# Performance work log

Measured on AMD Instinct MI355X. Metric: run time of the kernel, lower is better.

## Reference

```python
import jax, jax.numpy as jnp
import numpy as np

FEATURE_NUM = 2048
TEMPERATURE = 0.5
EPS = 1e-12


def setup_inputs() -> dict:
    key = jax.random.key(0)
    k1, k2 = jax.random.split(key)
    B, N = 8192, FEATURE_NUM
    f1 = jax.random.uniform(k1, (B, N), dtype=jnp.float32)
    f2 = jax.random.uniform(k2, (B, N), dtype=jnp.float32)
    return {"f1": f1, "f2": f2}


def reference(f1, f2):
    N = FEATURE_NUM
    K = 2 * N
    # rows = features, cols = batch samples
    f = jnp.concatenate([f1.T, f2.T], axis=0)  # [K, B]

    # normalized entropy loss (predictions are sigmoid outputs in (0,1))
    ent = -f * jnp.log(f + EPS) - (1.0 - f) * jnp.log(1.0 - f + EPS)
    neloss = jnp.mean(ent) / jnp.log(2.0)

    # L2 normalize rows (torch F.normalize: x / max(||x||, eps))
    norm = jnp.linalg.norm(f, axis=1, keepdims=True)
    fn = f / jnp.maximum(norm, EPS)

    sim = (fn @ fn.T) / TEMPERATURE  # [K, K]

    # positives: off-diagonals at +/- N
    pos = jnp.concatenate([jnp.diagonal(sim, N), jnp.diagonal(sim, -N)])  # [K]

    # logits per row = [pos, negatives]; negatives = row minus main diag and +/-N diag.
    # logsumexp(pos U negatives) == logsumexp over the row excluding only the main diagonal,
    # since pos IS the +/-N diagonal entry of that row.
    diag_mask = jnp.eye(K, dtype=bool)
    lse = jax.nn.logsumexp(jnp.where(diag_mask, -jnp.inf, sim), axis=1)  # [K]

    # cross-entropy with label 0 (the positive slot), mean reduction
    ce = jnp.mean(lse - pos)
    return ce - neloss
```

## Files before the change

### kernel.cpp

```cpp
#include <hip/hip_runtime.h>
#include <math.h>

typedef __attribute__((ext_vector_type(4))) float f32x4;
typedef __attribute__((ext_vector_type(8))) short short8;
typedef unsigned int u32;

#define B_DIM 8192
#define N_FEAT 2048
#define K_ROWS 4096
#define INV_T 2.0f
#define EPSF 1e-12f

#define GT 96
#define GGRID 43
#define NTILES 946

#define FT_OFF    0ull
#define NORM2_OFF 67108864ull
#define INV_OFF   (NORM2_OFF + 16384)
#define SUMSQ_OFF (INV_OFF + 16384)
#define RSUM_OFF  (SUMSQ_OFF + 16384)
#define PDOT_OFF  (RSUM_OFF + 16384)
#define ENT_OFF   (PDOT_OFF + 8192)
#define WS_END    (ENT_OFF + 2048)

__device__ __forceinline__ unsigned short f2bf(float x) {
  u32 u = __float_as_uint(x);
  u32 r = (u + 0x7fffu + ((u >> 16) & 1u)) >> 16;
  return (unsigned short)r;
}

__device__ __forceinline__ void gload16(const void* g, void* l) {
  __builtin_amdgcn_global_load_lds((const __attribute__((address_space(1))) u32*)g,
                                   (__attribute__((address_space(3))) u32*)l, 16, 0, 0);
}

__global__ __launch_bounds__(256) void stats_kernel(
    const float* __restrict__ f1, const float* __restrict__ f2,
    float* __restrict__ norm2, float* __restrict__ posdot,
    double* __restrict__ entpart) {
  const int col = blockIdx.x * 256 + threadIdx.x;
  const size_t base = (size_t)blockIdx.y * 64 * N_FEAT + col;
  const float* p1 = f1 + base;
  const float* p2 = f2 + base;
  float n1 = 0.f, n2 = 0.f, pd = 0.f, e0 = 0.f, e1 = 0.f;
#pragma unroll 8
  for (int r = 0; r < 64; ++r) {
    const float x = p1[(size_t)r * N_FEAT];
    const float y = p2[(size_t)r * N_FEAT];
    n1 += x * x; n2 += y * y; pd += x * y;
    e0 -= x * __log2f(x + EPSF) + (1.f - x) * __log2f(1.f - x + EPSF);
    e1 -= y * __log2f(y + EPSF) + (1.f - y) * __log2f(1.f - y + EPSF);
  }
  atomicAdd(&norm2[col], n1);
  atomicAdd(&norm2[N_FEAT + col], n2);
  atomicAdd(&posdot[col], pd);
  float ent = e0 + e1;
#pragma unroll
  for (int off = 1; off < 64; off <<= 1) ent += __shfl_xor(ent, off);
  if ((threadIdx.x & 63) == 0)
    atomicAdd(&entpart[(blockIdx.y * 8 + blockIdx.x + (threadIdx.x >> 6) * 64) & 255],
              (double)ent);
}

__global__ __launch_bounds__(256) void transpose_kernel(
    const float* __restrict__ f1, const float* __restrict__ f2,
    unsigned short* __restrict__ fT) {
  __shared__ float T1[64][65];
  __shared__ float T2[64][65];
  const int b0 = blockIdx.x * 64, k0 = blockIdx.y * 64;
  const int t = threadIdx.x;
  const int kq = t & 15, br = t >> 4;
#pragma unroll
  for (int rr = 0; rr < 4; ++rr) {
    const int b = br + rr * 16;
    const f32x4 v1 = *(const f32x4*)&f1[(size_t)(b0 + b) * N_FEAT + k0 + kq * 4];
    const f32x4 v2 = *(const f32x4*)&f2[(size_t)(b0 + b) * N_FEAT + k0 + kq * 4];
#pragma unroll
    for (int c = 0; c < 4; ++c) { T1[b][kq * 4 + c] = v1[c]; T2[b][kq * 4 + c] = v2[c]; }
  }
  __syncthreads();
  const int kl = t >> 2;
  const int b8 = (t & 3) * 16;
  short8 o0, o1;
#pragma unroll
  for (int j = 0; j < 8; ++j)  o0[j] = (short)f2bf(T1[b8 + j][kl]);
#pragma unroll
  for (int j = 8; j < 16; ++j) o1[j - 8] = (short)f2bf(T1[b8 + j][kl]);
  size_t gi = (size_t)(k0 + kl);
  *(short8*)&fT[gi * B_DIM + b0 + b8] = o0;
  *(short8*)&fT[gi * B_DIM + b0 + b8 + 8] = o1;
#pragma unroll
  for (int j = 0; j < 8; ++j)  o0[j] = (short)f2bf(T2[b8 + j][kl]);
#pragma unroll
  for (int j = 8; j < 16; ++j) o1[j - 8] = (short)f2bf(T2[b8 + j][kl]);
  gi = (size_t)(N_FEAT + k0 + kl);
  *(short8*)&fT[gi * B_DIM + b0 + b8] = o0;
  *(short8*)&fT[gi * B_DIM + b0 + b8 + 8] = o1;
}

__global__ void inv_kernel(const float* __restrict__ norm2, float* __restrict__ inv) {
  const int i = blockIdx.x * 256 + threadIdx.x;
  if (i < K_ROWS) inv[i] = 1.f / fmaxf(sqrtf(norm2[i]), EPSF);
}

__global__ __launch_bounds__(256, 4) void gram_kernel(
    const unsigned short* __restrict__ fT, const float* __restrict__ inv,
    float* __restrict__ rowsum) {
  __shared__ __align__(16) unsigned short Al[GT * 64];
  __shared__ __align__(16) unsigned short Bl[GT * 64];
  const int orig = blockIdx.x;
  const int xcd = orig & 7;
  const int bid = (xcd < 2 ? xcd * 119 : 238 + (xcd - 2) * 118) + (orig >> 3);
  int r = (int)((sqrtf(8.f * (float)bid + 1.f) - 1.f) * 0.5f);
  while ((r + 1) * (r + 2) / 2 <= bid) ++r;
  while (r * (r + 1) / 2 > bid) --r;
  const int tj = r, ti = bid - r * (r + 1) / 2;

  const int t = threadIdx.x, lane = t & 63, wave = t >> 6;
  const int wr = wave >> 1, wc = wave & 1;
  const int Rb = wr * 48, Cb = wc * 48;
  const int rowl = lane & 15, lhi = lane >> 4;
  const int srow8 = wave * 8 + (lane >> 3);
  const int scol = (lane & 7) * 8;
  const int tb = ti * GT, tjb = tj * GT;
  const bool diagT = (ti == tj);

  const unsigned short* pa[3];
  const unsigned short* pb[3];
#pragma unroll
  for (int it = 0; it < 3; ++it) {
    int ra = tb + it * 32 + srow8;  ra = ra < K_ROWS - 1 ? ra : K_ROWS - 1;
    int rb2 = tjb + it * 32 + srow8; rb2 = rb2 < K_ROWS - 1 ? rb2 : K_ROWS - 1;
    pa[it] = fT + (size_t)ra * B_DIM + scol;
    pb[it] = fT + (size_t)rb2 * B_DIM + scol;
  }

  f32x4 acc[3][3];
  const f32x4 zero = {0.f, 0.f, 0.f, 0.f};
#pragma unroll
  for (int m = 0; m < 3; ++m)
#pragma unroll
    for (int n = 0; n < 3; ++n) acc[m][n] = zero;

  for (int kt = 0; kt < B_DIM / 64; ++kt) {
    const size_t ko = (size_t)kt * 64;
#pragma unroll
    for (int it = 0; it < 3; ++it) {
      gload16(pa[it] + ko, &Al[(it * 32 + wave * 8) * 64]);
      gload16(pb[it] + ko, &Bl[(it * 32 + wave * 8) * 64]);
    }
    asm volatile("s_waitcnt vmcnt(0)" ::: "memory");
    __syncthreads();
#pragma unroll
    for (int kk = 0; kk < 64; kk += 32) {
      short8 af[3], bfv[3];
      const int kc = kk + lhi * 8;
#pragma unroll
      for (int m = 0; m < 3; ++m)
        af[m] = *(const short8*)&Al[(Rb + m * 16 + rowl) * 64 + kc];
#pragma unroll
      for (int n = 0; n < 3; ++n)
        bfv[n] = *(const short8*)&Bl[(Cb + n * 16 + rowl) * 64 + kc];
#pragma unroll
      for (int m = 0; m < 3; ++m)
#pragma unroll
        for (int n = 0; n < 3; ++n)
          acc[m][n] = __builtin_amdgcn_mfma_f32_16x16x32_bf16(af[m], bfv[n], acc[m][n], 0, 0, 0);
    }
    __syncthreads();
  }

  float invj[3];
  bool cval[3];
#pragma unroll
  for (int n = 0; n < 3; ++n) {
    const int cg = tjb + Cb + n * 16 + rowl;
    cval[n] = cg < K_ROWS;
    invj[n] = inv[cg < K_ROWS ? cg : K_ROWS - 1];
  }
#pragma unroll
  for (int m = 0; m < 3; ++m) {
#pragma unroll
    for (int rg = 0; rg < 4; ++rg) {
      const int rloc = Rb + m * 16 + lhi * 4 + rg;
      const int rgl = tb + rloc;
      const bool rv = rgl < K_ROWS;
      const float invi = inv[rv ? rgl : K_ROWS - 1];
#pragma unroll
      for (int n = 0; n < 3; ++n) {
        const int cloc = Cb + n * 16 + rowl;
        const float e = __expf(acc[m][n][rg] * invi * invj[n] * INV_T);
        const bool keep = rv && cval[n] && !(diagT && rloc == cloc);
        acc[m][n][rg] = keep ? e : 0.f;
      }
    }
  }
#pragma unroll
  for (int m = 0; m < 3; ++m) {
#pragma unroll
    for (int rg = 0; rg < 4; ++rg) {
      float s = acc[m][0][rg] + acc[m][1][rg] + acc[m][2][rg];
      s += __shfl_xor(s, 1); s += __shfl_xor(s, 2);
      s += __shfl_xor(s, 4); s += __shfl_xor(s, 8);
      if (rowl == 0) {
        const int rgl = tb + Rb + m * 16 + lhi * 4 + rg;
        if (rgl < K_ROWS) atomicAdd(&rowsum[rgl], s);
      }
    }
  }
  if (!diagT) {
#pragma unroll
    for (int n = 0; n < 3; ++n) {
      float s = 0.f;
#pragma unroll
      for (int m = 0; m < 3; ++m)
#pragma unroll
        for (int rg = 0; rg < 4; ++rg) s += acc[m][n][rg];
      s += __shfl_xor(s, 16); s += __shfl_xor(s, 32);
      if (lhi == 0) {
        const int cg = tjb + Cb + n * 16 + rowl;
        if (cg < K_ROWS) atomicAdd(&rowsum[cg], s);
      }
    }
  }
}

__global__ __launch_bounds__(256) void final_kernel(
    const float* __restrict__ rowsum,
    const float* __restrict__ inv, const float* __restrict__ posdot,
    const double* __restrict__ entpart, float* __restrict__ out) {
  __shared__ double red[4];
  __shared__ double rede[4];
  const int t = threadIdx.x, lane = t & 63, wave = t >> 6;
  double ssum = 0.0;
  for (int i = t; i < K_ROWS; i += 256) {
    const float invi = inv[i];
    const float lse = __logf(rowsum[i]);
    const int ip = (i < N_FEAT) ? i : i - N_FEAT;
    const int io = (i < N_FEAT) ? i + N_FEAT : i - N_FEAT;
    const float pos = posdot[ip] * invi * inv[io] * INV_T;
    ssum += (double)(lse - pos);
  }
  double esum = entpart[t];
#pragma unroll
  for (int off = 1; off < 64; off <<= 1) {
    ssum += __shfl_xor(ssum, off);
    esum += __shfl_xor(esum, off);
  }
  if (lane == 0) { red[wave] = ssum; rede[wave] = esum; }
  __syncthreads();
  if (t == 0) {
    const double ce = (red[0] + red[1] + red[2] + red[3]) / (double)K_ROWS;
    const double etot = rede[0] + rede[1] + rede[2] + rede[3];
    const double nel = etot / ((double)K_ROWS * (double)B_DIM);
    out[0] = (float)(ce - nel);
  }
}

extern "C" void kernel_launch(void* const* d_in, const int* in_sizes, int n_in,
                              void* d_out, int out_size, void* d_ws, size_t ws_size,
                              hipStream_t stream) {
  const float* f1 = (const float*)d_in[0];
  const float* f2 = (const float*)d_in[1];
  char* ws = (char*)d_ws;
  unsigned short* fT = (unsigned short*)(ws + FT_OFF);
  float* norm2 = (float*)(ws + NORM2_OFF);
  float* inv = (float*)(ws + INV_OFF);
  float* rowsum = (float*)(ws + RSUM_OFF);
  float* posdot = (float*)(ws + PDOT_OFF);
  double* entpart = (double*)(ws + ENT_OFF);

  hipMemsetAsync(ws + NORM2_OFF, 0, (size_t)(WS_END - NORM2_OFF), stream);

  stats_kernel<<<dim3(N_FEAT / 256, 128), 256, 0, stream>>>(f1, f2, norm2, posdot, entpart);
  inv_kernel<<<K_ROWS / 256, 256, 0, stream>>>(norm2, inv);
  transpose_kernel<<<dim3(B_DIM / 64, N_FEAT / 64), 256, 0, stream>>>(f1, f2, fT);
  gram_kernel<<<NTILES, 256, 0, stream>>>(fT, inv, rowsum);
  final_kernel<<<1, 256, 0, stream>>>(rowsum, inv, posdot, entpart, (float*)d_out);
}
```

Baseline: 392.3 us.

## Double-buffer LDS in gram kernel and widen transpose store pattern

The gram kernel now uses two LDS buffers so global-to-LDS loads for the next K-tile are issued before computing the current tile, overlapping memory latency with MFMA work and dropping one barrier per iteration. The transpose kernel's output stage is restructured so each thread writes 8 bf16 per row across two row groups, changing the LDS read and global store pattern. LDS usage doubles to about 48KB per block, which may reduce occupancy below the four blocks per CU the launch bounds request. An unused SUMSQ workspace slot is also folded away.

```diff
diff --git a/kernel.cpp b/kernel.cpp
--- a/kernel.cpp
+++ b/kernel.cpp
@@ -18,8 +18,7 @@
 #define FT_OFF    0ull
 #define NORM2_OFF 67108864ull
 #define INV_OFF   (NORM2_OFF + 16384)
-#define SUMSQ_OFF (INV_OFF + 16384)
-#define RSUM_OFF  (SUMSQ_OFF + 16384)
+#define RSUM_OFF  (INV_OFF + 32768)
 #define PDOT_OFF  (RSUM_OFF + 16384)
 #define ENT_OFF   (PDOT_OFF + 8192)
 #define WS_END    (ENT_OFF + 2048)
@@ -80,23 +79,19 @@
     for (int c = 0; c < 4; ++c) { T1[b][kq * 4 + c] = v1[c]; T2[b][kq * 4 + c] = v2[c]; }
   }
   __syncthreads();
-  const int kl = t >> 2;
-  const int b8 = (t & 3) * 16;
-  short8 o0, o1;
-#pragma unroll
-  for (int j = 0; j < 8; ++j)  o0[j] = (short)f2bf(T1[b8 + j][kl]);
-#pragma unroll
-  for (int j = 8; j < 16; ++j) o1[j - 8] = (short)f2bf(T1[b8 + j][kl]);
-  size_t gi = (size_t)(k0 + kl);
-  *(short8*)&fT[gi * B_DIM + b0 + b8] = o0;
-  *(short8*)&fT[gi * B_DIM + b0 + b8 + 8] = o1;
-#pragma unroll
-  for (int j = 0; j < 8; ++j)  o0[j] = (short)f2bf(T2[b8 + j][kl]);
-#pragma unroll
-  for (int j = 8; j < 16; ++j) o1[j - 8] = (short)f2bf(T2[b8 + j][kl]);
-  gi = (size_t)(N_FEAT + k0 + kl);
-  *(short8*)&fT[gi * B_DIM + b0 + b8] = o0;
-  *(short8*)&fT[gi * B_DIM + b0 + b8 + 8] = o1;
+  const int kl0 = t >> 3;
+  const int b8 = (t & 7) * 8;
+#pragma unroll
+  for (int rr = 0; rr < 2; ++rr) {
+    const int kl = rr * 32 + kl0;
+    short8 o;
+#pragma unroll
+    for (int j = 0; j < 8; ++j) o[j] = (short)f2bf(T1[b8 + j][kl]);
+    *(short8*)&fT[(size_t)(k0 + kl) * B_DIM + b0 + b8] = o;
+#pragma unroll
+    for (int j = 0; j < 8; ++j) o[j] = (short)f2bf(T2[b8 + j][kl]);
+    *(short8*)&fT[(size_t)(N_FEAT + k0 + kl) * B_DIM + b0 + b8] = o;
+  }
 }
 
 __global__ void inv_kernel(const float* __restrict__ norm2, float* __restrict__ inv) {
@@ -107,8 +102,8 @@
 __global__ __launch_bounds__(256, 4) void gram_kernel(
     const unsigned short* __restrict__ fT, const float* __restrict__ inv,
     float* __restrict__ rowsum) {
-  __shared__ __align__(16) unsigned short Al[GT * 64];
-  __shared__ __align__(16) unsigned short Bl[GT * 64];
+  __shared__ __align__(16) unsigned short Al[2][GT * 64];
+  __shared__ __align__(16) unsigned short Bl[2][GT * 64];
   const int orig = blockIdx.x;
   const int xcd = orig & 7;
   const int bid = (xcd < 2 ? xcd * 119 : 238 + (xcd - 2) * 118) + (orig >> 3);
@@ -143,33 +138,53 @@
 #pragma unroll
     for (int n = 0; n < 3; ++n) acc[m][n] = zero;
 
-  for (int kt = 0; kt < B_DIM / 64; ++kt) {
-    const size_t ko = (size_t)kt * 64;
-#pragma unroll
-    for (int it = 0; it < 3; ++it) {
-      gload16(pa[it] + ko, &Al[(it * 32 + wave * 8) * 64]);
-      gload16(pb[it] + ko, &Bl[(it * 32 + wave * 8) * 64]);
-    }
+#define STAGE(buf, kt)                                                        \
+  do {                                                                        \
+    const size_t ko_ = (size_t)(kt) * 64;                                     \
+    _Pragma("unroll")                                                         \
+    for (int it = 0; it < 3; ++it) {                                          \
+      gload16(pa[it] + ko_, &Al[buf][(it * 32 + wave * 8) * 64]);             \
+      gload16(pb[it] + ko_, &Bl[buf][(it * 32 + wave * 8) * 64]);             \
+    }                                                                         \
+  } while (0)
+
+#define COMPUTE(buf)                                                          \
+  do {                                                                        \
+    _Pragma("unroll")                                                         \
+    for (int kk = 0; kk < 64; kk += 32) {                                     \
+      short8 af[3], bfv[3];                                                   \
+      const int kc = kk + lhi * 8;                                            \
+      _Pragma("unroll")                                                       \
+      for (int m = 0; m < 3; ++m)                                             \
+        af[m] = *(const short8*)&Al[buf][(Rb + m * 16 + rowl) * 64 + kc];     \
+      _Pragma("unroll")                                                       \
+      for (int n = 0; n < 3; ++n)                                             \
+        bfv[n] = *(const short8*)&Bl[buf][(Cb + n * 16 + rowl) * 64 + kc];    \
+      _Pragma("unroll")                                                       \
+      for (int m = 0; m < 3; ++m)                                             \
+        _Pragma("unroll")                                                     \
+        for (int n = 0; n < 3; ++n)                                           \
+          acc[m][n] =                                                         \
+              __builtin_amdgcn_mfma_f32_16x16x32_bf16(af[m], bfv[n],          \
+                                                      acc[m][n], 0, 0, 0);    \
+    }                                                                         \
+  } while (0)
+
+  STAGE(0, 0);
+  asm volatile("s_waitcnt vmcnt(0)" ::: "memory");
+  __syncthreads();
+#pragma unroll 2
+  for (int kt = 0; kt < B_DIM / 64 - 1; ++kt) {
+    const int cur = kt & 1;
+    STAGE(cur ^ 1, kt + 1);
+    COMPUTE(cur);
     asm volatile("s_waitcnt vmcnt(0)" ::: "memory");
     __syncthreads();
-#pragma unroll
-    for (int kk = 0; kk < 64; kk += 32) {
-      short8 af[3], bfv[3];
-      const int kc = kk + lhi * 8;
-#pragma unroll
-      for (int m = 0; m < 3; ++m)
-        af[m] = *(const short8*)&Al[(Rb + m * 16 + rowl) * 64 + kc];
-#pragma unroll
-      for (int n = 0; n < 3; ++n)
-        bfv[n] = *(const short8*)&Bl[(Cb + n * 16 + rowl) * 64 + kc];
-#pragma unroll
-      for (int m = 0; m < 3; ++m)
-#pragma unroll
-        for (int n = 0; n < 3; ++n)
-          acc[m][n] = __builtin_amdgcn_mfma_f32_16x16x32_bf16(af[m], bfv[n], acc[m][n], 0, 0, 0);
-    }
-    __syncthreads();
-  }
+  }
+  COMPUTE((B_DIM / 64 - 1) & 1);
+
+#undef STAGE
+#undef COMPUTE
 
   float invj[3];
   bool cval[3];
```

Result: slower. 497.3 us (+26.8%).
